# Kernel optimization log

Hardware: AMD Instinct MI355X
Metric: run time of the kernel (lower is better)

The kernel has to match this reference:

```python
import jax, jax.numpy as jnp
import numpy as np

B, L, D_MODEL, N_HEADS = 4, 2048, 1024, 16
HEAD_DIM = D_MODEL // N_HEADS


def setup_inputs() -> dict:
    key = jax.random.key(0)
    ks = jax.random.split(key, 11)
    s = 1.0 / np.sqrt(D_MODEL)
    return {
        "queries": jax.random.normal(ks[0], (B, L, D_MODEL), jnp.float32),
        "keys": jax.random.normal(ks[1], (B, L, D_MODEL), jnp.float32),
        "values": jax.random.normal(ks[2], (B, L, D_MODEL), jnp.float32),
        "Wq": jax.random.normal(ks[3], (D_MODEL, D_MODEL), jnp.float32) * s,
        "bq": jnp.zeros((D_MODEL,), jnp.float32),
        "Wk": jax.random.normal(ks[4], (D_MODEL, D_MODEL), jnp.float32) * s,
        "bk": jnp.zeros((D_MODEL,), jnp.float32),
        "Wv": jax.random.normal(ks[5], (D_MODEL, D_MODEL), jnp.float32) * s,
        "bv": jnp.zeros((D_MODEL,), jnp.float32),
        "Wo": jax.random.normal(ks[6], (D_MODEL, D_MODEL), jnp.float32) * s,
        "bo": jnp.zeros((D_MODEL,), jnp.float32),
    }


def reference(queries, keys, values, Wq, bq, Wk, bk, Wv, bv, Wo, bo):
    Bsz, Lq, _ = queries.shape
    S = keys.shape[1]
    H, E = N_HEADS, HEAD_DIM
    # QKV projections (weights stored [in, out])
    q = (queries @ Wq + bq).reshape(Bsz, Lq, H, E)
    k = (keys @ Wk + bk).reshape(Bsz, S, H, E)
    v = (values @ Wv + bv).reshape(Bsz, S, H, E)
    scale = 1.0 / np.sqrt(E)
    # scores: [B, H, L, S]
    scores = jnp.einsum("blhe,bshe->bhls", q, k)
    A = jax.nn.softmax(scale * scores, axis=-1)
    # context: [B, L, H, E] -> [B, L, D]
    ctx = jnp.einsum("bhls,bshd->blhd", A, v).reshape(Bsz, Lq, H * E)
    out = ctx @ Wo + bo
    return out
```

## Files before the change

### kernel.cpp

```cpp
#include <hip/hip_runtime.h>

#define BATCH 4
#define SEQ   2048
#define DMODEL 1024
#define NHEADS 16
#define HDIM  64
#define MROWS (BATCH * SEQ)

typedef float f32x4 __attribute__((ext_vector_type(4)));
typedef short s16x8 __attribute__((ext_vector_type(8)));
typedef short s16x4 __attribute__((ext_vector_type(4)));
typedef unsigned short u16;

#define MFMA32K(a, b, c) __builtin_amdgcn_mfma_f32_16x16x32_bf16((a), (b), (c), 0, 0, 0)
#define MFMA16K(a, b, c) __builtin_amdgcn_mfma_f32_16x16x16bf16_1k((a), (b), (c), 0, 0, 0)

__device__ __forceinline__ u16 f2bf(float x) {
    unsigned int u = __builtin_bit_cast(unsigned int, x);
    unsigned int r = u + 0x7fffu + ((u >> 16) & 1u);
    return (u16)(r >> 16);
}

#if __has_builtin(__builtin_amdgcn_cvt_pk_bf16_f32)
__device__ __forceinline__ unsigned int pack2bf(float a, float b) {
    auto r = __builtin_amdgcn_cvt_pk_bf16_f32(a, b);
    return __builtin_bit_cast(unsigned int, r);
}
#else
__device__ __forceinline__ unsigned int pack2bf(float a, float b) {
    return (unsigned int)f2bf(a) | ((unsigned int)f2bf(b) << 16);
}
#endif

__device__ __forceinline__ void dma16(const u16* g, const u16* l) {
    __builtin_amdgcn_global_load_lds(
        (const __attribute__((address_space(1))) unsigned int*)g,
        (__attribute__((address_space(3))) unsigned int*)l, 16, 0, 0);
}

__global__ __launch_bounds__(256) void convk3(
    const float* __restrict__ s0, const float* __restrict__ s1,
    const float* __restrict__ s2, u16* __restrict__ d0, u16* __restrict__ d1,
    u16* __restrict__ d2) {
    const int z = blockIdx.y;
    const float* src = (z == 0) ? s0 : (z == 1) ? s1 : s2;
    u16* dst = (z == 0) ? d0 : (z == 1) ? d1 : d2;
    const int i = blockIdx.x * 256 + threadIdx.x;
    float4 a = ((const float4*)src)[i * 2];
    float4 b = ((const float4*)src)[i * 2 + 1];
    uint4 o;
    o.x = pack2bf(a.x, a.y); o.y = pack2bf(a.z, a.w);
    o.z = pack2bf(b.x, b.y); o.w = pack2bf(b.z, b.w);
    *(uint4*)(dst + (size_t)i * 8) = o;
}

__global__ __launch_bounds__(256) void wconv(const float* __restrict__ W0,
                                             const float* __restrict__ W1,
                                             const float* __restrict__ W2,
                                             const float* __restrict__ W3,
                                             u16* __restrict__ Wt) {
    __shared__ u16 tile[64][80];
    const int t = threadIdx.x;
    const int mtx = blockIdx.z;
    const float* W = (mtx == 0) ? W0 : (mtx == 1) ? W1 : (mtx == 2) ? W2 : W3;
    u16* out = Wt + (size_t)mtx * DMODEL * DMODEL;
    const int n0 = blockIdx.x * 64, k0 = blockIdx.y * 64;
#pragma unroll
    for (int j = 0; j < 4; ++j) {
        int k = j * 16 + (t >> 4);
        int c = (t & 15) * 4;
        float4 v = *(const float4*)(W + (size_t)(k0 + k) * DMODEL + n0 + c);
        tile[c + 0][k] = f2bf(v.x);
        tile[c + 1][k] = f2bf(v.y);
        tile[c + 2][k] = f2bf(v.z);
        tile[c + 3][k] = f2bf(v.w);
    }
    __syncthreads();
#pragma unroll
    for (int i2 = 0; i2 < 2; ++i2) {
        int n = i2 * 32 + (t >> 3), ck = (t & 7) * 8;
        uint4 v = *(const uint4*)(&tile[n][ck]);
        *(uint4*)(out + (size_t)(n0 + n) * DMODEL + k0 + ck) = v;
    }
}

__global__ __launch_bounds__(256) void gemm_qkv(
    const u16* __restrict__ Aq, const u16* __restrict__ Ak,
    const u16* __restrict__ Av, const u16* __restrict__ Wt,
    const float* __restrict__ biq, const float* __restrict__ bik,
    const float* __restrict__ biv, u16* __restrict__ oq, u16* __restrict__ ok,
    u16* __restrict__ ov, float sq) {
    __shared__ u16 As[128 * 32];
    __shared__ u16 Bs[128 * 32];
    const int t = threadIdx.x;
    const int w = t >> 6, lane = t & 63, quad = lane >> 4, l16 = lane & 15;
    const int z = blockIdx.z;
    const u16* A = (z == 0) ? Aq : (z == 1) ? Ak : Av;
    const u16* B = Wt + (size_t)z * DMODEL * DMODEL;
    const float* bias = (z == 0) ? biq : (z == 1) ? bik : biv;
    u16* C = (z == 0) ? oq : (z == 1) ? ok : ov;
    const float scale = (z == 0) ? sq : 1.0f;
    const int m0 = blockIdx.x * 128, n0 = blockIdx.y * 128;
    const int wm = (w >> 1) * 64, wn = (w & 1) * 64;
    const int lr = lane >> 2, lc = (lane & 3) * 8;

    f32x4 acc[4][4] = {};

    for (int k0 = 0; k0 < DMODEL; k0 += 32) {
#pragma unroll
        for (int j = 0; j < 2; ++j) {
            int row = w * 32 + j * 16;
            dma16(A + (size_t)(m0 + row + lr) * DMODEL + k0 + lc, &As[row * 32]);
            dma16(B + (size_t)(n0 + row + lr) * DMODEL + k0 + lc, &Bs[row * 32]);
        }
        __syncthreads();
        s16x8 af[4], bf[4];
#pragma unroll
        for (int mt = 0; mt < 4; ++mt)
            af[mt] = *(const s16x8*)(&As[(wm + mt * 16 + l16) * 32 + quad * 8]);
#pragma unroll
        for (int nt = 0; nt < 4; ++nt)
            bf[nt] = *(const s16x8*)(&Bs[(wn + nt * 16 + l16) * 32 + quad * 8]);
#pragma unroll
        for (int mt = 0; mt < 4; ++mt)
#pragma unroll
            for (int nt = 0; nt < 4; ++nt)
                acc[mt][nt] = MFMA32K(af[mt], bf[nt], acc[mt][nt]);
        __syncthreads();
    }

#pragma unroll
    for (int mt = 0; mt < 4; ++mt)
#pragma unroll
        for (int nt = 0; nt < 4; ++nt) {
            int col = n0 + wn + nt * 16 + l16;
            float bv_ = bias[col];
#pragma unroll
            for (int r = 0; r < 4; ++r) {
                int row = m0 + wm + mt * 16 + quad * 4 + r;
                C[(size_t)row * DMODEL + col] = f2bf((acc[mt][nt][r] + bv_) * scale);
            }
        }
}

__global__ __launch_bounds__(256) void gemm_o(const u16* __restrict__ A,
                                              const u16* __restrict__ Bt,
                                              const float* __restrict__ bias,
                                              float* __restrict__ Cp) {
    __shared__ u16 As[128 * 32];
    __shared__ u16 Bs[128 * 32];
    const int t = threadIdx.x;
    const int w = t >> 6, lane = t & 63, quad = lane >> 4, l16 = lane & 15;
    const int m0 = blockIdx.x * 128, n0 = blockIdx.y * 128;
    const int wm = (w >> 1) * 64, wn = (w & 1) * 64;
    const int lr = lane >> 2, lc = (lane & 3) * 8;

    f32x4 acc[4][4] = {};

    for (int k0 = 0; k0 < DMODEL; k0 += 32) {
#pragma unroll
        for (int j = 0; j < 2; ++j) {
            int row = w * 32 + j * 16;
            dma16(A + (size_t)(m0 + row + lr) * DMODEL + k0 + lc, &As[row * 32]);
            dma16(Bt + (size_t)(n0 + row + lr) * DMODEL + k0 + lc, &Bs[row * 32]);
        }
        __syncthreads();
        s16x8 af[4], bf[4];
#pragma unroll
        for (int mt = 0; mt < 4; ++mt)
            af[mt] = *(const s16x8*)(&As[(wm + mt * 16 + l16) * 32 + quad * 8]);
#pragma unroll
        for (int nt = 0; nt < 4; ++nt)
            bf[nt] = *(const s16x8*)(&Bs[(wn + nt * 16 + l16) * 32 + quad * 8]);
#pragma unroll
        for (int mt = 0; mt < 4; ++mt)
#pragma unroll
            for (int nt = 0; nt < 4; ++nt)
                acc[mt][nt] = MFMA32K(af[mt], bf[nt], acc[mt][nt]);
        __syncthreads();
    }

#pragma unroll
    for (int mt = 0; mt < 4; ++mt)
#pragma unroll
        for (int nt = 0; nt < 4; ++nt) {
            int col = n0 + wn + nt * 16 + l16;
            float bv_ = bias[col];
#pragma unroll
            for (int r = 0; r < 4; ++r) {
                int row = m0 + wm + mt * 16 + quad * 4 + r;
                Cp[(size_t)row * DMODEL + col] = acc[mt][nt][r] + bv_;
            }
        }
}

__global__ __launch_bounds__(256) void attn3(const u16* __restrict__ qb,
                                             const u16* __restrict__ kb,
                                             const u16* __restrict__ vb,
                                             u16* __restrict__ ctxb) {
    __shared__ u16 Ks[64 * 64];
    __shared__ u16 Vt[64 * 72];
    const int t = threadIdx.x;
    const int w = t >> 6, lane = t & 63, quad = lane >> 4, l16 = lane & 15;
    const int h = blockIdx.x, b = blockIdx.z, q0 = blockIdx.y * 128;

    s16x8 bq[2][2];
#pragma unroll
    for (int qs = 0; qs < 2; ++qs) {
        size_t base = (size_t)(b * SEQ + q0 + w * 32 + qs * 16 + l16) * DMODEL + h * HDIM + quad * 8;
        bq[qs][0] = *(const s16x8*)(qb + base);
        bq[qs][1] = *(const s16x8*)(qb + base + 32);
    }

    const int krow = lane >> 3;
    const int kunit = (lane & 7) ^ (krow & 7);

    float lsum[2] = {0.0f, 0.0f};
    f32x4 o[2][4] = {};

    for (int s0 = 0; s0 < SEQ; s0 += 64) {
        __syncthreads();
#pragma unroll
        for (int j = 0; j < 2; ++j) {
            int row = w * 16 + j * 8 + krow;
            dma16(kb + (size_t)(b * SEQ + s0 + row) * DMODEL + h * HDIM + kunit * 8,
                  &Ks[(w * 16 + j * 8) * 64]);
        }
#pragma unroll
        for (int i = 0; i < 2; ++i) {
            int idx = i * 256 + t;
            int key = idx >> 3, seg = idx & 7;
            union { uint4 v; u16 s[8]; } u;
            u.v = *(const uint4*)(vb + (size_t)(b * SEQ + s0 + key) * DMODEL + h * HDIM + seg * 8);
            int col = (((key >> 3) ^ seg) << 3) + (key & 7);
#pragma unroll
            for (int ii = 0; ii < 8; ++ii)
                Vt[(seg * 8 + ii) * 72 + col] = u.s[ii];
        }
        __syncthreads();

        s16x8 ak[4][2];
#pragma unroll
        for (int kt = 0; kt < 4; ++kt) {
            int row = kt * 16 + l16;
#pragma unroll
            for (int hf = 0; hf < 2; ++hf) {
                int un = (hf * 4 + quad) ^ (l16 & 7);
                ak[kt][hf] = *(const s16x8*)(&Ks[row * 64 + un * 8]);
            }
        }

        unsigned int pk[2][4][2];
#pragma unroll
        for (int qs = 0; qs < 2; ++qs) {
            f32x4 sc[4];
#pragma unroll
            for (int kt = 0; kt < 4; ++kt) {
                f32x4 zz = {0.0f, 0.0f, 0.0f, 0.0f};
                zz = MFMA32K(ak[kt][0], bq[qs][0], zz);
                sc[kt] = MFMA32K(ak[kt][1], bq[qs][1], zz);
            }
            float rs = 0.0f;
            float p[4][4];
#pragma unroll
            for (int kt = 0; kt < 4; ++kt)
#pragma unroll
                for (int r = 0; r < 4; ++r) {
                    p[kt][r] = __builtin_amdgcn_exp2f(sc[kt][r]);
                    rs += p[kt][r];
                }
            rs += __shfl_xor(rs, 16);
            rs += __shfl_xor(rs, 32);
            lsum[qs] += rs;
#pragma unroll
            for (int kt = 0; kt < 4; ++kt) {
                pk[qs][kt][0] = pack2bf(p[kt][0], p[kt][1]);
                pk[qs][kt][1] = pack2bf(p[kt][2], p[kt][3]);
            }
        }

#pragma unroll
        for (int mt = 0; mt < 4; ++mt) {
            const int dim = mt * 16 + l16;
            const int swz = (dim >> 3) & 7;
            const int rowoff = dim * 72;
#pragma unroll
            for (int kt = 0; kt < 4; ++kt) {
                int col = ((((kt * 2) + (quad >> 1)) ^ swz) << 3) + ((quad & 1) << 2);
                s16x4 av = *(const s16x4*)(&Vt[rowoff + col]);
#pragma unroll
                for (int qs = 0; qs < 2; ++qs) {
                    union { unsigned int u[2]; s16x4 v; } pb;
                    pb.u[0] = pk[qs][kt][0];
                    pb.u[1] = pk[qs][kt][1];
                    o[qs][mt] = MFMA16K(av, pb.v, o[qs][mt]);
                }
            }
        }
    }

#pragma unroll
    for (int qs = 0; qs < 2; ++qs) {
        float rl = 1.0f / lsum[qs];
        size_t rowbase = (size_t)(b * SEQ + q0 + w * 32 + qs * 16 + l16) * DMODEL + h * HDIM;
#pragma unroll
        for (int mt = 0; mt < 4; ++mt)
#pragma unroll
            for (int rr = 0; rr < 2; ++rr) {
                unsigned int v = pack2bf(o[qs][mt][rr * 2] * rl, o[qs][mt][rr * 2 + 1] * rl);
                *(unsigned int*)(&ctxb[rowbase + mt * 16 + quad * 4 + rr * 2]) = v;
            }
    }
}

extern "C" void kernel_launch(void* const* d_in, const int* in_sizes, int n_in,
                              void* d_out, int out_size, void* d_ws, size_t ws_size,
                              hipStream_t stream) {
    const float* queries = (const float*)d_in[0];
    const float* keys    = (const float*)d_in[1];
    const float* values  = (const float*)d_in[2];
    const float* Wq = (const float*)d_in[3];
    const float* bq = (const float*)d_in[4];
    const float* Wk = (const float*)d_in[5];
    const float* bk = (const float*)d_in[6];
    const float* Wv = (const float*)d_in[7];
    const float* bv = (const float*)d_in[8];
    const float* Wo = (const float*)d_in[9];
    const float* bo = (const float*)d_in[10];
    float* out = (float*)d_out;

    char* ws = (char*)d_ws;
    u16* Wt   = (u16*)ws;
    u16* aq   = (u16*)(ws + ((size_t)8 << 20));
    u16* ak   = (u16*)(ws + ((size_t)24 << 20));
    u16* av   = (u16*)(ws + ((size_t)40 << 20));
    u16* qbuf = (u16*)(ws + ((size_t)56 << 20));
    u16* kbuf = (u16*)(ws + ((size_t)72 << 20));
    u16* vbuf = (u16*)(ws + ((size_t)88 << 20));
    u16* ctxb = qbuf;

    const size_t WSZ = (size_t)DMODEL * DMODEL;
    const float S2 = 0.125f * 1.44269504088896340736f;

    dim3 blk(256);

    wconv<<<dim3(16, 16, 4), blk, 0, stream>>>(Wq, Wk, Wv, Wo, Wt);
    convk3<<<dim3(4096, 3), blk, 0, stream>>>(queries, keys, values, aq, ak, av);

    gemm_qkv<<<dim3(64, 8, 3), blk, 0, stream>>>(aq, ak, av, Wt,
                                                 bq, bk, bv, qbuf, kbuf, vbuf, S2);

    attn3<<<dim3(NHEADS, SEQ / 128, BATCH), blk, 0, stream>>>(qbuf, kbuf, vbuf, ctxb);

    gemm_o<<<dim3(64, 8), blk, 0, stream>>>(ctxb, Wt + 3 * WSZ, bo, out);
}
```

Measured before the change: 373.2 us.

## Pre-transpose V globally and double-buffer K/V tiles with async DMA in attention

Adds a separate kernel that writes V transposed per head to a global buffer, reusing the freed input-activation workspace. The attention kernel can then stage both K and V tiles with async direct-to-LDS copies instead of scalar transposing stores. It also double-buffers those tiles so the next tile loads while the current one computes, and raises MFMA priority via s_setprio. The cost is an extra kernel launch, one more read and write pass over V, and double the LDS per block.

```diff
diff --git a/kernel.cpp b/kernel.cpp
--- a/kernel.cpp
+++ b/kernel.cpp
@@ -84,6 +84,31 @@
     }
 }
 
+__global__ __launch_bounds__(256) void vtrans(const u16* __restrict__ vbuf,
+                                              u16* __restrict__ vtg) {
+    __shared__ u16 tile[64][72];
+    const int t = threadIdx.x;
+    const int s0 = blockIdx.x * 64, h = blockIdx.y, b = blockIdx.z;
+#pragma unroll
+    for (int i = 0; i < 2; ++i) {
+        int idx = i * 256 + t;
+        int srow = idx >> 3, un = idx & 7;
+        union { uint4 v; u16 s[8]; } u;
+        u.v = *(const uint4*)(vbuf + (size_t)(b * SEQ + s0 + srow) * DMODEL + h * HDIM + un * 8);
+#pragma unroll
+        for (int ii = 0; ii < 8; ++ii)
+            tile[un * 8 + ii][srow] = u.s[ii];
+    }
+    __syncthreads();
+#pragma unroll
+    for (int i = 0; i < 2; ++i) {
+        int idx = i * 256 + t;
+        int e = idx >> 3, un = idx & 7;
+        uint4 v = *(const uint4*)(&tile[e][un * 8]);
+        *(uint4*)(vtg + ((size_t)((b * NHEADS + h) * HDIM + e)) * SEQ + s0 + un * 8) = v;
+    }
+}
+
 __global__ __launch_bounds__(256) void gemm_qkv(
     const u16* __restrict__ Aq, const u16* __restrict__ Ak,
     const u16* __restrict__ Av, const u16* __restrict__ Wt,
@@ -194,12 +219,12 @@
         }
 }
 
-__global__ __launch_bounds__(256) void attn3(const u16* __restrict__ qb,
-                                             const u16* __restrict__ kb,
-                                             const u16* __restrict__ vb,
-                                             u16* __restrict__ ctxb) {
-    __shared__ u16 Ks[64 * 64];
-    __shared__ u16 Vt[64 * 72];
+__global__ __launch_bounds__(256, 4) void attn3(const u16* __restrict__ qb,
+                                                const u16* __restrict__ kb,
+                                                const u16* __restrict__ vtg,
+                                                u16* __restrict__ ctxb) {
+    __shared__ u16 Ks[2][64 * 64];
+    __shared__ u16 Vt[2][64 * 64];
     const int t = threadIdx.x;
     const int w = t >> 6, lane = t & 63, quad = lane >> 4, l16 = lane & 15;
     const int h = blockIdx.x, b = blockIdx.z, q0 = blockIdx.y * 128;
@@ -213,31 +238,31 @@
     }
 
     const int krow = lane >> 3;
-    const int kunit = (lane & 7) ^ (krow & 7);
+    const int kunit = (lane & 7) ^ krow;
+    const u16* vbase = vtg + (size_t)((b * NHEADS + h) * HDIM) * SEQ;
 
     float lsum[2] = {0.0f, 0.0f};
     f32x4 o[2][4] = {};
 
-    for (int s0 = 0; s0 < SEQ; s0 += 64) {
-        __syncthreads();
-#pragma unroll
-        for (int j = 0; j < 2; ++j) {
-            int row = w * 16 + j * 8 + krow;
-            dma16(kb + (size_t)(b * SEQ + s0 + row) * DMODEL + h * HDIM + kunit * 8,
-                  &Ks[(w * 16 + j * 8) * 64]);
-        }
-#pragma unroll
-        for (int i = 0; i < 2; ++i) {
-            int idx = i * 256 + t;
-            int key = idx >> 3, seg = idx & 7;
-            union { uint4 v; u16 s[8]; } u;
-            u.v = *(const uint4*)(vb + (size_t)(b * SEQ + s0 + key) * DMODEL + h * HDIM + seg * 8);
-            int col = (((key >> 3) ^ seg) << 3) + (key & 7);
-#pragma unroll
-            for (int ii = 0; ii < 8; ++ii)
-                Vt[(seg * 8 + ii) * 72 + col] = u.s[ii];
-        }
-        __syncthreads();
+#define STAGE_KV(bf_, ss_)                                                              \
+    do {                                                                                \
+        _Pragma("unroll")                                                               \
+        for (int j = 0; j < 2; ++j) {                                                   \
+            int row = w * 16 + j * 8 + krow;                                            \
+            dma16(kb + (size_t)(b * SEQ + (ss_) + row) * DMODEL + h * HDIM + kunit * 8, \
+                  &Ks[bf_][(w * 16 + j * 8) * 64]);                                     \
+            dma16(vbase + (size_t)row * SEQ + (ss_) + kunit * 8,                        \
+                  &Vt[bf_][(w * 16 + j * 8) * 64]);                                     \
+        }                                                                               \
+    } while (0)
+
+    STAGE_KV(0, 0);
+    __syncthreads();
+
+    const int NT = SEQ / 64;
+    for (int tt = 0; tt < NT; ++tt) {
+        const int buf = tt & 1;
+        if (tt + 1 < NT) STAGE_KV(buf ^ 1, (tt + 1) * 64);
 
         s16x8 ak[4][2];
 #pragma unroll
@@ -246,20 +271,22 @@
 #pragma unroll
             for (int hf = 0; hf < 2; ++hf) {
                 int un = (hf * 4 + quad) ^ (l16 & 7);
-                ak[kt][hf] = *(const s16x8*)(&Ks[row * 64 + un * 8]);
-            }
-        }
-
-        unsigned int pk[2][4][2];
+                ak[kt][hf] = *(const s16x8*)(&Ks[buf][row * 64 + un * 8]);
+            }
+        }
+
+        s16x4 pf[2][4];
 #pragma unroll
         for (int qs = 0; qs < 2; ++qs) {
             f32x4 sc[4];
+            __builtin_amdgcn_s_setprio(1);
 #pragma unroll
             for (int kt = 0; kt < 4; ++kt) {
                 f32x4 zz = {0.0f, 0.0f, 0.0f, 0.0f};
                 zz = MFMA32K(ak[kt][0], bq[qs][0], zz);
                 sc[kt] = MFMA32K(ak[kt][1], bq[qs][1], zz);
             }
+            __builtin_amdgcn_s_setprio(0);
             float rs = 0.0f;
             float p[4][4];
 #pragma unroll
@@ -274,30 +301,32 @@
             lsum[qs] += rs;
 #pragma unroll
             for (int kt = 0; kt < 4; ++kt) {
-                pk[qs][kt][0] = pack2bf(p[kt][0], p[kt][1]);
-                pk[qs][kt][1] = pack2bf(p[kt][2], p[kt][3]);
+                union { unsigned int u[2]; s16x4 v; } pb;
+                pb.u[0] = pack2bf(p[kt][0], p[kt][1]);
+                pb.u[1] = pack2bf(p[kt][2], p[kt][3]);
+                pf[qs][kt] = pb.v;
             }
         }
 
 #pragma unroll
         for (int mt = 0; mt < 4; ++mt) {
             const int dim = mt * 16 + l16;
-            const int swz = (dim >> 3) & 7;
-            const int rowoff = dim * 72;
+            const u16* vrow = &Vt[buf][dim * 64 + ((quad & 1) << 2)];
+            const int sw = l16 & 7;
 #pragma unroll
             for (int kt = 0; kt < 4; ++kt) {
-                int col = ((((kt * 2) + (quad >> 1)) ^ swz) << 3) + ((quad & 1) << 2);
-                s16x4 av = *(const s16x4*)(&Vt[rowoff + col]);
-#pragma unroll
-                for (int qs = 0; qs < 2; ++qs) {
-                    union { unsigned int u[2]; s16x4 v; } pb;
-                    pb.u[0] = pk[qs][kt][0];
-                    pb.u[1] = pk[qs][kt][1];
-                    o[qs][mt] = MFMA16K(av, pb.v, o[qs][mt]);
-                }
-            }
-        }
-    }
+                int un = (kt * 2 + (quad >> 1)) ^ sw;
+                s16x4 av = *(const s16x4*)(vrow + un * 8);
+                __builtin_amdgcn_s_setprio(1);
+#pragma unroll
+                for (int qs = 0; qs < 2; ++qs)
+                    o[qs][mt] = MFMA16K(av, pf[qs][kt], o[qs][mt]);
+                __builtin_amdgcn_s_setprio(0);
+            }
+        }
+        __syncthreads();
+    }
+#undef STAGE_KV
 
 #pragma unroll
     for (int qs = 0; qs < 2; ++qs) {
@@ -338,6 +367,7 @@
     u16* kbuf = (u16*)(ws + ((size_t)72 << 20));
     u16* vbuf = (u16*)(ws + ((size_t)88 << 20));
     u16* ctxb = qbuf;
+    u16* vtg  = av;
 
     const size_t WSZ = (size_t)DMODEL * DMODEL;
     const float S2 = 0.125f * 1.44269504088896340736f;
@@ -350,7 +380,9 @@
     gemm_qkv<<<dim3(64, 8, 3), blk, 0, stream>>>(aq, ak, av, Wt,
                                                  bq, bk, bv, qbuf, kbuf, vbuf, S2);
 
-    attn3<<<dim3(NHEADS, SEQ / 128, BATCH), blk, 0, stream>>>(qbuf, kbuf, vbuf, ctxb);
+    vtrans<<<dim3(SEQ / 64, NHEADS, BATCH), blk, 0, stream>>>(vbuf, vtg);
+
+    attn3<<<dim3(NHEADS, SEQ / 128, BATCH), blk, 0, stream>>>(qbuf, kbuf, vtg, ctxb);
 
     gemm_o<<<dim3(64, 8), blk, 0, stream>>>(ctxb, Wt + 3 * WSZ, bo, out);
 }
```

After: 425.5 us. +14.0%, slower.

## Merge conversion kernels and use K=64 tiles with XOR-swizzled LDS in GEMMs

Applied to the files above, without the earlier changes.

Fuses the activation and weight fp32-to-bf16 conversion kernels into one launch so there is one fewer kernel launch. Both projection GEMMs now stage 64-wide K slices, which halves the number of barrier pairs per tile. The LDS layout is XOR-swizzled by row so the 16-byte fragment reads avoid bank conflicts. In exchange, LDS use doubles to 32KB per block, which may lower occupancy.

```diff
diff --git a/kernel.cpp b/kernel.cpp
--- a/kernel.cpp
+++ b/kernel.cpp
@@ -38,49 +38,50 @@
         (__attribute__((address_space(3))) unsigned int*)l, 16, 0, 0);
 }
 
-__global__ __launch_bounds__(256) void convk3(
+__global__ __launch_bounds__(256) void prep(
     const float* __restrict__ s0, const float* __restrict__ s1,
     const float* __restrict__ s2, u16* __restrict__ d0, u16* __restrict__ d1,
-    u16* __restrict__ d2) {
-    const int z = blockIdx.y;
-    const float* src = (z == 0) ? s0 : (z == 1) ? s1 : s2;
-    u16* dst = (z == 0) ? d0 : (z == 1) ? d1 : d2;
-    const int i = blockIdx.x * 256 + threadIdx.x;
-    float4 a = ((const float4*)src)[i * 2];
-    float4 b = ((const float4*)src)[i * 2 + 1];
-    uint4 o;
-    o.x = pack2bf(a.x, a.y); o.y = pack2bf(a.z, a.w);
-    o.z = pack2bf(b.x, b.y); o.w = pack2bf(b.z, b.w);
-    *(uint4*)(dst + (size_t)i * 8) = o;
-}
-
-__global__ __launch_bounds__(256) void wconv(const float* __restrict__ W0,
-                                             const float* __restrict__ W1,
-                                             const float* __restrict__ W2,
-                                             const float* __restrict__ W3,
-                                             u16* __restrict__ Wt) {
+    u16* __restrict__ d2, const float* __restrict__ W0,
+    const float* __restrict__ W1, const float* __restrict__ W2,
+    const float* __restrict__ W3, u16* __restrict__ Wt) {
     __shared__ u16 tile[64][80];
+    const int bid = blockIdx.x;
     const int t = threadIdx.x;
-    const int mtx = blockIdx.z;
-    const float* W = (mtx == 0) ? W0 : (mtx == 1) ? W1 : (mtx == 2) ? W2 : W3;
-    u16* out = Wt + (size_t)mtx * DMODEL * DMODEL;
-    const int n0 = blockIdx.x * 64, k0 = blockIdx.y * 64;
-#pragma unroll
-    for (int j = 0; j < 4; ++j) {
-        int k = j * 16 + (t >> 4);
-        int c = (t & 15) * 4;
-        float4 v = *(const float4*)(W + (size_t)(k0 + k) * DMODEL + n0 + c);
-        tile[c + 0][k] = f2bf(v.x);
-        tile[c + 1][k] = f2bf(v.y);
-        tile[c + 2][k] = f2bf(v.z);
-        tile[c + 3][k] = f2bf(v.w);
-    }
-    __syncthreads();
-#pragma unroll
-    for (int i2 = 0; i2 < 2; ++i2) {
-        int n = i2 * 32 + (t >> 3), ck = (t & 7) * 8;
-        uint4 v = *(const uint4*)(&tile[n][ck]);
-        *(uint4*)(out + (size_t)(n0 + n) * DMODEL + k0 + ck) = v;
+    if (bid < 12288) {
+        const int z = bid >> 12, xi = bid & 4095;
+        const float* src = (z == 0) ? s0 : (z == 1) ? s1 : s2;
+        u16* dst = (z == 0) ? d0 : (z == 1) ? d1 : d2;
+        const int i = xi * 256 + t;
+        float4 a = ((const float4*)src)[i * 2];
+        float4 b = ((const float4*)src)[i * 2 + 1];
+        uint4 o;
+        o.x = pack2bf(a.x, a.y); o.y = pack2bf(a.z, a.w);
+        o.z = pack2bf(b.x, b.y); o.w = pack2bf(b.z, b.w);
+        *(uint4*)(dst + (size_t)i * 8) = o;
+    } else {
+        const int wb = bid - 12288;
+        const int mtx = wb >> 8;
+        const int rem = wb & 255;
+        const float* W = (mtx == 0) ? W0 : (mtx == 1) ? W1 : (mtx == 2) ? W2 : W3;
+        u16* out = Wt + (size_t)mtx * DMODEL * DMODEL;
+        const int n0 = (rem & 15) * 64, k0 = (rem >> 4) * 64;
+#pragma unroll
+        for (int j = 0; j < 4; ++j) {
+            int k = j * 16 + (t >> 4);
+            int c = (t & 15) * 4;
+            float4 v = *(const float4*)(W + (size_t)(k0 + k) * DMODEL + n0 + c);
+            tile[c + 0][k] = f2bf(v.x);
+            tile[c + 1][k] = f2bf(v.y);
+            tile[c + 2][k] = f2bf(v.z);
+            tile[c + 3][k] = f2bf(v.w);
+        }
+        __syncthreads();
+#pragma unroll
+        for (int i2 = 0; i2 < 2; ++i2) {
+            int n = i2 * 32 + (t >> 3), ck = (t & 7) * 8;
+            uint4 v = *(const uint4*)(&tile[n][ck]);
+            *(uint4*)(out + (size_t)(n0 + n) * DMODEL + k0 + ck) = v;
+        }
     }
 }
 
@@ -90,8 +91,8 @@
     const float* __restrict__ biq, const float* __restrict__ bik,
     const float* __restrict__ biv, u16* __restrict__ oq, u16* __restrict__ ok,
     u16* __restrict__ ov, float sq) {
-    __shared__ u16 As[128 * 32];
-    __shared__ u16 Bs[128 * 32];
+    __shared__ u16 As[128 * 64];
+    __shared__ u16 Bs[128 * 64];
     const int t = threadIdx.x;
     const int w = t >> 6, lane = t & 63, quad = lane >> 4, l16 = lane & 15;
     const int z = blockIdx.z;
@@ -102,30 +103,34 @@
     const float scale = (z == 0) ? sq : 1.0f;
     const int m0 = blockIdx.x * 128, n0 = blockIdx.y * 128;
     const int wm = (w >> 1) * 64, wn = (w & 1) * 64;
-    const int lr = lane >> 2, lc = (lane & 3) * 8;
+    const int lr8 = lane >> 3;
+    const int lun = (lane & 7) ^ lr8;
 
     f32x4 acc[4][4] = {};
 
-    for (int k0 = 0; k0 < DMODEL; k0 += 32) {
-#pragma unroll
-        for (int j = 0; j < 2; ++j) {
-            int row = w * 32 + j * 16;
-            dma16(A + (size_t)(m0 + row + lr) * DMODEL + k0 + lc, &As[row * 32]);
-            dma16(B + (size_t)(n0 + row + lr) * DMODEL + k0 + lc, &Bs[row * 32]);
-        }
-        __syncthreads();
-        s16x8 af[4], bf[4];
-#pragma unroll
-        for (int mt = 0; mt < 4; ++mt)
-            af[mt] = *(const s16x8*)(&As[(wm + mt * 16 + l16) * 32 + quad * 8]);
-#pragma unroll
-        for (int nt = 0; nt < 4; ++nt)
-            bf[nt] = *(const s16x8*)(&Bs[(wn + nt * 16 + l16) * 32 + quad * 8]);
-#pragma unroll
-        for (int mt = 0; mt < 4; ++mt)
-#pragma unroll
-            for (int nt = 0; nt < 4; ++nt)
-                acc[mt][nt] = MFMA32K(af[mt], bf[nt], acc[mt][nt]);
+    for (int k0 = 0; k0 < DMODEL; k0 += 64) {
+#pragma unroll
+        for (int j = 0; j < 4; ++j) {
+            int r8 = w * 32 + j * 8;
+            dma16(A + (size_t)(m0 + r8 + lr8) * DMODEL + k0 + lun * 8, &As[r8 * 64]);
+            dma16(B + (size_t)(n0 + r8 + lr8) * DMODEL + k0 + lun * 8, &Bs[r8 * 64]);
+        }
+        __syncthreads();
+#pragma unroll
+        for (int half = 0; half < 2; ++half) {
+            s16x8 af[4], bf[4];
+#pragma unroll
+            for (int mt = 0; mt < 4; ++mt) {
+                int un = ((half * 4 + quad) ^ (l16 & 7)) * 8;
+                af[mt] = *(const s16x8*)(&As[(wm + mt * 16 + l16) * 64 + un]);
+                bf[mt] = *(const s16x8*)(&Bs[(wn + mt * 16 + l16) * 64 + un]);
+            }
+#pragma unroll
+            for (int mt = 0; mt < 4; ++mt)
+#pragma unroll
+                for (int nt = 0; nt < 4; ++nt)
+                    acc[mt][nt] = MFMA32K(af[mt], bf[nt], acc[mt][nt]);
+        }
         __syncthreads();
     }
 
@@ -147,36 +152,40 @@
                                               const u16* __restrict__ Bt,
                                               const float* __restrict__ bias,
                                               float* __restrict__ Cp) {
-    __shared__ u16 As[128 * 32];
-    __shared__ u16 Bs[128 * 32];
+    __shared__ u16 As[128 * 64];
+    __shared__ u16 Bs[128 * 64];
     const int t = threadIdx.x;
     const int w = t >> 6, lane = t & 63, quad = lane >> 4, l16 = lane & 15;
     const int m0 = blockIdx.x * 128, n0 = blockIdx.y * 128;
     const int wm = (w >> 1) * 64, wn = (w & 1) * 64;
-    const int lr = lane >> 2, lc = (lane & 3) * 8;
+    const int lr8 = lane >> 3;
+    const int lun = (lane & 7) ^ lr8;
 
     f32x4 acc[4][4] = {};
 
-    for (int k0 = 0; k0 < DMODEL; k0 += 32) {
-#pragma unroll
-        for (int j = 0; j < 2; ++j) {
-            int row = w * 32 + j * 16;
-            dma16(A + (size_t)(m0 + row + lr) * DMODEL + k0 + lc, &As[row * 32]);
-            dma16(Bt + (size_t)(n0 + row + lr) * DMODEL + k0 + lc, &Bs[row * 32]);
-        }
-        __syncthreads();
-        s16x8 af[4], bf[4];
-#pragma unroll
-        for (int mt = 0; mt < 4; ++mt)
-            af[mt] = *(const s16x8*)(&As[(wm + mt * 16 + l16) * 32 + quad * 8]);
-#pragma unroll
-        for (int nt = 0; nt < 4; ++nt)
-            bf[nt] = *(const s16x8*)(&Bs[(wn + nt * 16 + l16) * 32 + quad * 8]);
-#pragma unroll
-        for (int mt = 0; mt < 4; ++mt)
-#pragma unroll
-            for (int nt = 0; nt < 4; ++nt)
-                acc[mt][nt] = MFMA32K(af[mt], bf[nt], acc[mt][nt]);
+    for (int k0 = 0; k0 < DMODEL; k0 += 64) {
+#pragma unroll
+        for (int j = 0; j < 4; ++j) {
+            int r8 = w * 32 + j * 8;
+            dma16(A + (size_t)(m0 + r8 + lr8) * DMODEL + k0 + lun * 8, &As[r8 * 64]);
+            dma16(Bt + (size_t)(n0 + r8 + lr8) * DMODEL + k0 + lun * 8, &Bs[r8 * 64]);
+        }
+        __syncthreads();
+#pragma unroll
+        for (int half = 0; half < 2; ++half) {
+            s16x8 af[4], bf[4];
+#pragma unroll
+            for (int mt = 0; mt < 4; ++mt) {
+                int un = ((half * 4 + quad) ^ (l16 & 7)) * 8;
+                af[mt] = *(const s16x8*)(&As[(wm + mt * 16 + l16) * 64 + un]);
+                bf[mt] = *(const s16x8*)(&Bs[(wn + mt * 16 + l16) * 64 + un]);
+            }
+#pragma unroll
+            for (int mt = 0; mt < 4; ++mt)
+#pragma unroll
+                for (int nt = 0; nt < 4; ++nt)
+                    acc[mt][nt] = MFMA32K(af[mt], bf[nt], acc[mt][nt]);
+        }
         __syncthreads();
     }
 
@@ -344,8 +353,8 @@
 
     dim3 blk(256);
 
-    wconv<<<dim3(16, 16, 4), blk, 0, stream>>>(Wq, Wk, Wv, Wo, Wt);
-    convk3<<<dim3(4096, 3), blk, 0, stream>>>(queries, keys, values, aq, ak, av);
+    prep<<<dim3(13312), blk, 0, stream>>>(queries, keys, values, aq, ak, av,
+                                          Wq, Wk, Wv, Wo, Wt);
 
     gemm_qkv<<<dim3(64, 8, 3), blk, 0, stream>>>(aq, ak, av, Wt,
                                                  bq, bk, bv, qbuf, kbuf, vbuf, S2);
```

Measured after the change: 365.5 us. -2.1%, faster.
